# Kernel optimization log

Hardware: AMD Instinct MI355X
Metric: run time of the kernel (lower is better)

## Reference

```python
import jax, jax.numpy as jnp
import numpy as np

D_MODEL = 1024
N_HEADS = 16
DEPTH = D_MODEL // N_HEADS  # 64
BATCH, SEQ = 4, 2048


def setup_inputs() -> dict:
    key = jax.random.key(0)
    ks = jax.random.split(key, 8)
    x = jax.random.normal(ks[0], (BATCH, SEQ, D_MODEL), dtype=jnp.float32)
    # Per-head Dense(depth) weights stacked over heads: [H, d_model, depth]
    s = 1.0 / np.sqrt(D_MODEL)
    Wq = jax.random.normal(ks[1], (N_HEADS, D_MODEL, DEPTH), dtype=jnp.float32) * s
    Wk = jax.random.normal(ks[2], (N_HEADS, D_MODEL, DEPTH), dtype=jnp.float32) * s
    Wv = jax.random.normal(ks[3], (N_HEADS, D_MODEL, DEPTH), dtype=jnp.float32) * s
    bq = jnp.zeros((N_HEADS, DEPTH), dtype=jnp.float32)
    bk = jnp.zeros((N_HEADS, DEPTH), dtype=jnp.float32)
    bv = jnp.zeros((N_HEADS, DEPTH), dtype=jnp.float32)
    Wo = jax.random.normal(ks[4], (D_MODEL, D_MODEL), dtype=jnp.float32) * s
    bo = jnp.zeros((D_MODEL,), dtype=jnp.float32)
    return {"x": x, "Wq": Wq, "bq": bq, "Wk": Wk, "bk": bk,
            "Wv": Wv, "bv": bv, "Wo": Wo, "bo": bo}


def reference(x, Wq, bq, Wk, bk, Wv, bv, Wo, bo):
    # Per-head projections, batched over heads: [b, h, s, depth]
    q = jnp.einsum('bsd,hde->bhse', x, Wq) + bq[None, :, None, :]
    k = jnp.einsum('bsd,hde->bhse', x, Wk) + bk[None, :, None, :]
    v = jnp.einsum('bsd,hde->bhse', x, Wv) + bv[None, :, None, :]
    scale = 1.0 / jnp.sqrt(jnp.float32(DEPTH))
    scores = jnp.einsum('bhqe,bhke->bhqk', q, k) * scale  # [b, h, s, s]
    attn = jax.nn.softmax(scores, axis=-1)
    z = jnp.einsum('bhqk,bhke->bhqe', attn, v)  # [b, h, s, depth]
    # Concat heads along last axis (head-major order matches tf.concat of per-head outputs)
    multi_head = z.transpose(0, 2, 1, 3).reshape(BATCH, SEQ, D_MODEL)
    return multi_head @ Wo + bo
```

## Files before the change

kernel.cpp:

```cpp
#include <hip/hip_runtime.h>

typedef unsigned short u16;
typedef __bf16 bf16x8 __attribute__((ext_vector_type(8)));
typedef float f32x4 __attribute__((ext_vector_type(4)));
typedef float f32x16 __attribute__((ext_vector_type(16)));
typedef unsigned int u32x4 __attribute__((ext_vector_type(4)));
typedef unsigned int u32x2 __attribute__((ext_vector_type(2)));

__device__ __forceinline__ u16 f2b(float f) {
  union { float f; unsigned u; } v; v.f = f;
  return (u16)((v.u + 0x7fffu + ((v.u >> 16) & 1u)) >> 16);
}

__device__ __forceinline__ unsigned pkbf(float a, float b) {
#if __has_builtin(__builtin_amdgcn_cvt_pk_bf16_f32)
  typedef __bf16 bf16x2v __attribute__((ext_vector_type(2)));
  bf16x2v r = __builtin_amdgcn_cvt_pk_bf16_f32(a, b);
  return __builtin_bit_cast(unsigned, r);
#else
  unsigned ua = __builtin_bit_cast(unsigned, a) + 0x8000u;
  unsigned ub = __builtin_bit_cast(unsigned, b) + 0x8000u;
  return __builtin_amdgcn_perm(ub, ua, 0x07060302u);
#endif
}

__device__ __forceinline__ float fexp2(float x) {
#if __has_builtin(__builtin_amdgcn_exp2f)
  return __builtin_amdgcn_exp2f(x);
#else
  return exp2f(x);
#endif
}

__device__ __forceinline__ bf16x8 ldfrag(const u16* p) {
  u32x4 r = *(const u32x4*)p;
  return __builtin_bit_cast(bf16x8, r);
}

__device__ __forceinline__ void plswap(unsigned& dst, unsigned& src) {
  asm("v_permlane32_swap_b32 %0, %1" : "+v"(dst), "+v"(src));
}

__device__ __forceinline__ float sum16(const f32x16& v) {
  float a = (v[0] + v[1]) + (v[2] + v[3]);
  float b = (v[4] + v[5]) + (v[6] + v[7]);
  float c = (v[8] + v[9]) + (v[10] + v[11]);
  float d = (v[12] + v[13]) + (v[14] + v[15]);
  return (a + b) + (c + d);
}

__device__ __forceinline__ void build_frags(const f32x16& sc, bf16x8& fLo, bf16x8& fHi) {
  unsigned a0 = pkbf(sc[0], sc[1]);
  unsigned a1 = pkbf(sc[2], sc[3]);
  unsigned b0 = pkbf(sc[4], sc[5]);
  unsigned b1 = pkbf(sc[6], sc[7]);
  plswap(a0, b0);
  plswap(a1, b1);
  u32x4 f; f[0] = a0; f[1] = a1; f[2] = b0; f[3] = b1;
  fLo = __builtin_bit_cast(bf16x8, f);
  unsigned c0 = pkbf(sc[8], sc[9]);
  unsigned c1 = pkbf(sc[10], sc[11]);
  unsigned d0 = pkbf(sc[12], sc[13]);
  unsigned d1 = pkbf(sc[14], sc[15]);
  plswap(c0, d0);
  plswap(c1, d1);
  u32x4 g; g[0] = c0; g[1] = c1; g[2] = d0; g[3] = d1;
  fHi = __builtin_bit_cast(bf16x8, g);
}

#define GLOAD_LDS16(gp, lp)                                                        \
  __builtin_amdgcn_global_load_lds((const __attribute__((address_space(1))) void*)(gp), \
                                   (__attribute__((address_space(3))) void*)(lp), 16, 0, 0)

#define MFMA32(a, b, c) __builtin_amdgcn_mfma_f32_32x32x16_bf16((a), (b), (c), 0, 0, 0)

#define QSC 0.18033688011f


__global__ __launch_bounds__(256) void k_pack(const float* __restrict__ x,
                                              const float* __restrict__ Wq,
                                              const float* __restrict__ Wk,
                                              const float* __restrict__ Wv,
                                              const float* __restrict__ Wo,
                                              u16* __restrict__ xb,
                                              u16* __restrict__ wqkv,
                                              u16* __restrict__ wo_t) {
  const int bid = blockIdx.x, tid = threadIdx.x;
  if (bid < 4096) {
    int i = (bid * 256 + tid) * 8;
    float4 v0 = *(const float4*)(x + i);
    float4 v1 = *(const float4*)(x + i + 4);
    u32x4 o;
    o[0] = pkbf(v0.x, v0.y);
    o[1] = pkbf(v0.z, v0.w);
    o[2] = pkbf(v1.x, v1.y);
    o[3] = pkbf(v1.z, v1.w);
    *(u32x4*)(xb + i) = o;
    return;
  }
  __shared__ u16 tile[64][65];
  if (bid < 4864) {
    int b2 = bid - 4096;
    int p = b2 >> 8, rem = b2 & 255, h = rem >> 4, dt = rem & 15;
    const float* W = (p == 0) ? Wq : (p == 1) ? Wk : Wv;
    for (int i = tid; i < 4096; i += 256) {
      int d = i >> 6, e = i & 63;
      tile[e][d] = f2b(W[h * 65536 + (dt * 64 + d) * 64 + e]);
    }
    __syncthreads();
    for (int i = tid; i < 4096; i += 256) {
      int e = i >> 6, d = i & 63;
      wqkv[(size_t)(p * 1024 + h * 64 + e) * 1024 + dt * 64 + d] = tile[e][d];
    }
  } else {
    int b2 = bid - 4864;
    int kt = b2 >> 4, nt = b2 & 15;
    for (int i = tid; i < 4096; i += 256) {
      int dk = i >> 6, de = i & 63;
      tile[de][dk] = f2b(Wo[(size_t)(kt * 64 + dk) * 1024 + nt * 64 + de]);
    }
    __syncthreads();
    for (int i = tid; i < 4096; i += 256) {
      int de = i >> 6, dk = i & 63;
      wo_t[(size_t)(nt * 64 + de) * 1024 + kt * 64 + dk] = tile[de][dk];
    }
  }
}


template <bool SWAP>
__device__ __forceinline__ void gemm_core64(const u16* __restrict__ A, const u16* __restrict__ Bt,
                                            int row0, int col0, u16* As, u16* Bs, f32x16 acc[2][2]) {
  const int tid = threadIdx.x, w = tid >> 6, lane = tid & 63;
  const int l31 = lane & 31, hi = lane >> 5;
  const int wm = (w >> 1) * 64, wn = (w & 1) * 64;

  int r_[4], c_[4];
#pragma unroll
  for (int i = 0; i < 4; i++) {
    int E = (w * 4 + i) * 512 + lane * 8;
    int e = E ^ (((E >> 7) & 7) << 3);
    r_[i] = e >> 6;
    c_[i] = e & 63;
  }
  int oa[2][2][2], ob[2][2][2];
#pragma unroll
  for (int kh = 0; kh < 2; kh++)
#pragma unroll
    for (int t = 0; t < 2; t++)
#pragma unroll
      for (int s = 0; s < 2; s++) {
        int Pa = (wm + t * 32 + l31) * 64 + kh * 32 + s * 16 + hi * 8;
        int Pb = (wn + t * 32 + l31) * 64 + kh * 32 + s * 16 + hi * 8;
        oa[kh][t][s] = Pa ^ (((Pa >> 7) & 7) << 3);
        ob[kh][t][s] = Pb ^ (((Pb >> 7) & 7) << 3);
      }

  const u16* Ag = A + (size_t)row0 * 1024;
  const u16* Bg = Bt + (size_t)col0 * 1024;

#pragma unroll
  for (int i = 0; i < 4; i++) {
    GLOAD_LDS16(Ag + (size_t)r_[i] * 1024 + c_[i], As + (w * 4 + i) * 512);
    GLOAD_LDS16(Bg + (size_t)r_[i] * 1024 + c_[i], Bs + (w * 4 + i) * 512);
  }
  __syncthreads();

  int cur = 0;
  for (int k0 = 0; k0 < 1024; k0 += 64) {
    if (k0 + 64 < 1024) {
      u16* Ad = As + (cur ^ 1) * 8192 + (w * 4) * 512;
      u16* Bd = Bs + (cur ^ 1) * 8192 + (w * 4) * 512;
#pragma unroll
      for (int i = 0; i < 4; i++) {
        GLOAD_LDS16(Ag + (size_t)r_[i] * 1024 + k0 + 64 + c_[i], Ad + i * 512);
        GLOAD_LDS16(Bg + (size_t)r_[i] * 1024 + k0 + 64 + c_[i], Bd + i * 512);
      }
    }
    const u16* Ab = As + cur * 8192;
    const u16* Bb = Bs + cur * 8192;
#pragma unroll
    for (int kh = 0; kh < 2; kh++) {
      bf16x8 af[2][2], bfr[2][2];
#pragma unroll
      for (int t = 0; t < 2; t++)
#pragma unroll
        for (int s = 0; s < 2; s++) {
          af[t][s] = ldfrag(Ab + oa[kh][t][s]);
          bfr[t][s] = ldfrag(Bb + ob[kh][t][s]);
        }
      __builtin_amdgcn_s_setprio(1);
#pragma unroll
      for (int mt = 0; mt < 2; mt++)
#pragma unroll
        for (int nt = 0; nt < 2; nt++)
#pragma unroll
          for (int s = 0; s < 2; s++)
            acc[mt][nt] = SWAP ? MFMA32(bfr[nt][s], af[mt][s], acc[mt][nt])
                               : MFMA32(af[mt][s], bfr[nt][s], acc[mt][nt]);
      __builtin_amdgcn_s_setprio(0);
    }
    __syncthreads();
    cur ^= 1;
  }
}


__global__ __launch_bounds__(256) void k_gemm_qkv(const u16* __restrict__ xb, const u16* __restrict__ wt,
                                                  const float* __restrict__ bq, const float* __restrict__ bk,
                                                  const float* __restrict__ bv,
                                                  u16* __restrict__ qo, u16* __restrict__ ko,
                                                  u16* __restrict__ vto) {
  __shared__ u16 As[16384], Bs[16384];
  f32x16 acc[2][2];
#pragma unroll
  for (int a = 0; a < 2; a++)
#pragma unroll
    for (int b = 0; b < 2; b++)
#pragma unroll
      for (int r = 0; r < 16; r++) acc[a][b][r] = 0.f;

  const int row0 = blockIdx.x * 128, col0 = blockIdx.y * 128;
  const int p = blockIdx.y >> 3;
  const int colr = (blockIdx.y & 7) * 128;
  const int tid = threadIdx.x, w = tid >> 6, lane = tid & 63;
  const int l31 = lane & 31, hi = lane >> 5;
  const int wm = (w >> 1) * 64, wn = (w & 1) * 64;

  if (p == 2) {
    gemm_core64<true>(xb, wt, row0, col0, As, Bs, acc);
#pragma unroll
    for (int mt = 0; mt < 2; mt++) {
      int rb = row0 + wm + mt * 32;
      int b_ = rb >> 11;
      int s_ = (rb & 2047) + l31;
#pragma unroll
      for (int nt = 0; nt < 2; nt++) {
        int ebase = colr + wn + nt * 32;
#pragma unroll
        for (int g = 0; g < 4; g++) {
          float4 bvv = *(const float4*)(bv + ebase + g * 8 + hi * 4);
#pragma unroll
          for (int j = 0; j < 4; j++) {
            int rem = ebase + g * 8 + hi * 4 + j;
            int h = rem >> 6, e = rem & 63;
            float val = acc[mt][nt][g * 4 + j] + (&bvv.x)[j];
            vto[(((size_t)(b_ * 16 + h)) * 64 + e) * 2048 + s_] = f2b(val);
          }
        }
      }
    }
  } else {
    gemm_core64<false>(xb, wt, row0, col0, As, Bs, acc);
    u16* dst = (p == 0) ? qo : ko;
    const float* bias = (p == 0) ? bq : bk;
    const float qsc = (p == 0) ? QSC : 1.0f;
#pragma unroll
    for (int nt = 0; nt < 2; nt++) {
      int rem = colr + wn + nt * 32 + l31;
      int h = rem >> 6, e = rem & 63;
      float bval = bias[rem];
#pragma unroll
      for (int mt = 0; mt < 2; mt++) {
        int rb = row0 + wm + mt * 32;
        int b_ = rb >> 11, sb = rb & 2047;
        size_t obase = ((size_t)(b_ * 16 + h) * 2048) * 64 + e;
#pragma unroll
        for (int reg = 0; reg < 16; reg++) {
          int s_ = sb + (reg & 3) + 8 * (reg >> 2) + 4 * hi;
          float val = (acc[mt][nt][reg] + bval) * qsc;
          dst[obase + (size_t)s_ * 64] = f2b(val);
        }
      }
    }
  }
}


__global__ __launch_bounds__(256) void k_gemm_out(const u16* __restrict__ zb, const u16* __restrict__ wt,
                                                  const float* __restrict__ bo, float* __restrict__ out) {
  __shared__ u16 As[16384], Bs[16384];
  f32x16 acc[2][2];
#pragma unroll
  for (int a = 0; a < 2; a++)
#pragma unroll
    for (int b = 0; b < 2; b++)
#pragma unroll
      for (int r = 0; r < 16; r++) acc[a][b][r] = 0.f;

  const int row0 = blockIdx.x * 128, col0 = blockIdx.y * 128;
  gemm_core64<false>(zb, wt, row0, col0, As, Bs, acc);

  const int tid = threadIdx.x, w = tid >> 6, lane = tid & 63;
  const int l31 = lane & 31, hi = lane >> 5;
  const int wm = (w >> 1) * 64, wn = (w & 1) * 64;
#pragma unroll
  for (int nt = 0; nt < 2; nt++) {
    int c = col0 + wn + nt * 32 + l31;
    float bval = bo[c];
#pragma unroll
    for (int mt = 0; mt < 2; mt++) {
      int rb = row0 + wm + mt * 32;
#pragma unroll
      for (int reg = 0; reg < 16; reg++) {
        int r = rb + (reg & 3) + 8 * (reg >> 2) + 4 * hi;
        out[(size_t)r * 1024 + c] = acc[mt][nt][reg] + bval;
      }
    }
  }
}


__global__ __launch_bounds__(256, 2) void k_attn(const u16* __restrict__ q, const u16* __restrict__ k,
                                                 const u16* __restrict__ vt, u16* __restrict__ z) {
  __shared__ u16 Ks[2][64 * 72], Vs[2][64 * 72];
  const int tid = threadIdx.x, w = tid >> 6, lane = tid & 63;
  const int l31 = lane & 31, hi = lane >> 5;
  const int bh = blockIdx.x, s0 = blockIdx.y * 256;
  const size_t base = (size_t)bh * 2048 * 64;
  const int qrow0 = s0 + w * 64;

  bf16x8 qf[2][4];
#pragma unroll
  for (int u = 0; u < 2; u++) {
    const u16* qp = q + base + (size_t)(qrow0 + u * 32 + l31) * 64 + hi * 8;
#pragma unroll
    for (int ks = 0; ks < 4; ks++) qf[u][ks] = ldfrag(qp + ks * 16);
  }

  f32x16 accT[2][2];
  float ls[2] = {0.f, 0.f};
#pragma unroll
  for (int u = 0; u < 2; u++)
#pragma unroll
    for (int r = 0; r < 16; r++) { accT[u][0][r] = 0.f; accT[u][1][r] = 0.f; }

  const int srow = tid >> 3;
  const int scol = (tid & 7) * 8;
  const u16* kg = k + base;
  const u16* vg = vt + base;

  u32x4 kr0 = *(const u32x4*)(kg + (size_t)srow * 64 + scol);
  u32x4 kr1 = *(const u32x4*)(kg + (size_t)(srow + 32) * 64 + scol);
  u32x4 vr0 = *(const u32x4*)(vg + (size_t)srow * 2048 + scol);
  u32x4 vr1 = *(const u32x4*)(vg + (size_t)(srow + 32) * 2048 + scol);
  *(u32x4*)&Ks[0][srow * 72 + scol] = kr0;
  *(u32x4*)&Ks[0][(srow + 32) * 72 + scol] = kr1;
  *(u32x4*)&Vs[0][srow * 72 + scol] = vr0;
  *(u32x4*)&Vs[0][(srow + 32) * 72 + scol] = vr1;
  kr0 = *(const u32x4*)(kg + (size_t)(64 + srow) * 64 + scol);
  kr1 = *(const u32x4*)(kg + (size_t)(64 + srow + 32) * 64 + scol);
  vr0 = *(const u32x4*)(vg + (size_t)srow * 2048 + 64 + scol);
  vr1 = *(const u32x4*)(vg + (size_t)(srow + 32) * 2048 + 64 + scol);
  __syncthreads();

  for (int kc = 0; kc < 2048; kc += 64) {
    const int buf = (kc >> 6) & 1;
    const u16* Kb = &Ks[buf][0];
    const u16* Vb = &Vs[buf][0];

    bf16x8 pf[2][4];
#pragma unroll
    for (int t = 0; t < 2; t++) {
      f32x16 scA, scB;
#pragma unroll
      for (int r = 0; r < 16; r++) { scA[r] = 0.f; scB[r] = 0.f; }
      __builtin_amdgcn_s_setprio(1);
#pragma unroll
      for (int ks = 0; ks < 4; ks++) {
        bf16x8 kf = ldfrag(Kb + (t * 32 + l31) * 72 + ks * 16 + hi * 8);
        scA = MFMA32(kf, qf[0][ks], scA);
        scB = MFMA32(kf, qf[1][ks], scB);
      }
      __builtin_amdgcn_s_setprio(0);
#pragma unroll
      for (int r = 0; r < 16; r++) scA[r] = fexp2(scA[r]);
#pragma unroll
      for (int r = 0; r < 16; r++) scB[r] = fexp2(scB[r]);
      ls[0] += sum16(scA);
      ls[1] += sum16(scB);
      build_frags(scA, pf[0][2 * t], pf[0][2 * t + 1]);
      build_frags(scB, pf[1][2 * t], pf[1][2 * t + 1]);
    }

    if (kc + 64 < 2048) {
      *(u32x4*)&Ks[buf ^ 1][srow * 72 + scol] = kr0;
      *(u32x4*)&Ks[buf ^ 1][(srow + 32) * 72 + scol] = kr1;
      *(u32x4*)&Vs[buf ^ 1][srow * 72 + scol] = vr0;
      *(u32x4*)&Vs[buf ^ 1][(srow + 32) * 72 + scol] = vr1;
      if (kc + 128 < 2048) {
        int kn = kc + 128;
        kr0 = *(const u32x4*)(kg + (size_t)(kn + srow) * 64 + scol);
        kr1 = *(const u32x4*)(kg + (size_t)(kn + srow + 32) * 64 + scol);
        vr0 = *(const u32x4*)(vg + (size_t)srow * 2048 + kn + scol);
        vr1 = *(const u32x4*)(vg + (size_t)(srow + 32) * 2048 + kn + scol);
      }
    }

    __builtin_amdgcn_s_setprio(1);
#pragma unroll
    for (int ks = 0; ks < 4; ks++) {
      bf16x8 vf0 = ldfrag(Vb + (0 * 32 + l31) * 72 + ks * 16 + hi * 8);
      bf16x8 vf1 = ldfrag(Vb + (1 * 32 + l31) * 72 + ks * 16 + hi * 8);
      accT[0][0] = MFMA32(vf0, pf[0][ks], accT[0][0]);
      accT[0][1] = MFMA32(vf1, pf[0][ks], accT[0][1]);
      accT[1][0] = MFMA32(vf0, pf[1][ks], accT[1][0]);
      accT[1][1] = MFMA32(vf1, pf[1][ks], accT[1][1]);
    }
    __builtin_amdgcn_s_setprio(0);
    __syncthreads();
  }

  const int b_ = bh >> 4, h = bh & 15;
#pragma unroll
  for (int u = 0; u < 2; u++) {
    float l = ls[u];
    l += __shfl_xor(l, 32);
    float inv = 1.f / l;
    int qrow = qrow0 + u * 32 + l31;
    u16* zr = z + ((size_t)(b_ * 2048 + qrow)) * 1024 + h * 64;
#pragma unroll
    for (int et = 0; et < 2; et++)
#pragma unroll
      for (int rr = 0; rr < 16; rr += 2) {
        unsigned pkd = pkbf(accT[u][et][rr] * inv, accT[u][et][rr + 1] * inv);
        int e = et * 32 + (rr & 3) + 8 * (rr >> 2) + 4 * hi;
        *(unsigned*)&zr[e] = pkd;
      }
  }
}


extern "C" void kernel_launch(void* const* d_in, const int* in_sizes, int n_in,
                              void* d_out, int out_size, void* d_ws, size_t ws_size,
                              hipStream_t stream) {
  (void)in_sizes; (void)n_in; (void)out_size;
  const float* x  = (const float*)d_in[0];
  const float* Wq = (const float*)d_in[1];
  const float* bq = (const float*)d_in[2];
  const float* Wk = (const float*)d_in[3];
  const float* bk = (const float*)d_in[4];
  const float* Wv = (const float*)d_in[5];
  const float* bv = (const float*)d_in[6];
  const float* Wo = (const float*)d_in[7];
  const float* bo = (const float*)d_in[8];
  float* out = (float*)d_out;
  char* ws = (char*)d_ws;
  if (ws_size < 92274688u) return;

  u16* xb   = (u16*)(ws + 0);
  u16* wqkv = (u16*)(ws + 16777216);
  u16* wo_t = (u16*)(ws + 23068672);
  u16* qb   = (u16*)(ws + 25165824);
  u16* kb   = (u16*)(ws + 41943040);
  u16* vtb  = (u16*)(ws + 58720256);
  u16* zb   = (u16*)(ws + 75497472);

  k_pack<<<5120, 256, 0, stream>>>(x, Wq, Wk, Wv, Wo, xb, wqkv, wo_t);
  k_gemm_qkv<<<dim3(64, 24), 256, 0, stream>>>(xb, wqkv, bq, bk, bv, qb, kb, vtb);
  k_attn<<<dim3(64, 8), 256, 0, stream>>>(qb, kb, vtb, zb);
  k_gemm_out<<<dim3(64, 8), 256, 0, stream>>>(zb, wo_t, bo, out);
}
```

Baseline: 269.7 us.

## Stage K/V via direct global-to-LDS loads with pre-swizzled layout and 128-key tiles

The QKV projection now writes Q, K and transposed V with an XOR swizzle baked into global memory. The attention kernel can then copy K/V tiles straight into LDS with global-load-to-LDS instructions, with no padding and no register staging. The key tile grows from 64 to 128 per barrier, which halves the number of syncs and doubles LDS use to 64KB per block. This is meant to cut VGPR pressure, LDS store instructions and bank conflicts, but it may reduce occupancy and depends on the GLOAD_LDS16 macro defined elsewhere.

```diff
diff --git a/kernel.cpp b/kernel.cpp
--- a/kernel.cpp
+++ b/kernel.cpp
@@ -244,8 +244,9 @@
           for (int j = 0; j < 4; j++) {
             int rem = ebase + g * 8 + hi * 4 + j;
             int h = rem >> 6, e = rem & 63;
+            int e7 = (hi * 4 + j) & 7;
             float val = acc[mt][nt][g * 4 + j] + (&bvv.x)[j];
-            vto[(((size_t)(b_ * 16 + h)) * 64 + e) * 2048 + s_] = f2b(val);
+            vto[((size_t)(b_ * 16 + h) * 64 + e) * 2048 + (s_ ^ (e7 << 3))] = f2b(val);
           }
         }
       }
@@ -264,12 +265,14 @@
       for (int mt = 0; mt < 2; mt++) {
         int rb = row0 + wm + mt * 32;
         int b_ = rb >> 11, sb = rb & 2047;
-        size_t obase = ((size_t)(b_ * 16 + h) * 2048) * 64 + e;
+        size_t base2 = (size_t)(b_ * 16 + h) * 2048 * 64;
 #pragma unroll
         for (int reg = 0; reg < 16; reg++) {
-          int s_ = sb + (reg & 3) + 8 * (reg >> 2) + 4 * hi;
+          int low = (reg & 3) + 4 * hi + 8 * (reg >> 2);
+          int s_ = sb + low;
+          int esw = e ^ ((((low >> 1) & 7)) << 3);
           float val = (acc[mt][nt][reg] + bval) * qsc;
-          dst[obase + (size_t)s_ * 64] = f2b(val);
+          dst[base2 + (size_t)s_ * 64 + esw] = f2b(val);
         }
       }
     }
@@ -313,19 +316,21 @@
 
 __global__ __launch_bounds__(256, 2) void k_attn(const u16* __restrict__ q, const u16* __restrict__ k,
                                                  const u16* __restrict__ vt, u16* __restrict__ z) {
-  __shared__ u16 Ks[2][64 * 72], Vs[2][64 * 72];
+  __shared__ u16 Ks[2][128 * 64], Vs[2][64 * 128];
   const int tid = threadIdx.x, w = tid >> 6, lane = tid & 63;
   const int l31 = lane & 31, hi = lane >> 5;
   const int bh = blockIdx.x, s0 = blockIdx.y * 256;
   const size_t base = (size_t)bh * 2048 * 64;
   const int qrow0 = s0 + w * 64;
+  const int qx = ((l31 >> 1) & 7) << 3;
+  const int vx = (l31 & 7) << 3;
 
   bf16x8 qf[2][4];
 #pragma unroll
   for (int u = 0; u < 2; u++) {
-    const u16* qp = q + base + (size_t)(qrow0 + u * 32 + l31) * 64 + hi * 8;
-#pragma unroll
-    for (int ks = 0; ks < 4; ks++) qf[u][ks] = ldfrag(qp + ks * 16);
+    const u16* qp = q + base + (size_t)(qrow0 + u * 32 + l31) * 64;
+#pragma unroll
+    for (int ks = 0; ks < 4; ks++) qf[u][ks] = ldfrag(qp + ((ks * 16 + hi * 8) ^ qx));
   }
 
   f32x16 accT[2][2];
@@ -335,81 +340,70 @@
 #pragma unroll
     for (int r = 0; r < 16; r++) { accT[u][0][r] = 0.f; accT[u][1][r] = 0.f; }
 
-  const int srow = tid >> 3;
-  const int scol = (tid & 7) * 8;
   const u16* kg = k + base;
   const u16* vg = vt + base;
 
-  u32x4 kr0 = *(const u32x4*)(kg + (size_t)srow * 64 + scol);
-  u32x4 kr1 = *(const u32x4*)(kg + (size_t)(srow + 32) * 64 + scol);
-  u32x4 vr0 = *(const u32x4*)(vg + (size_t)srow * 2048 + scol);
-  u32x4 vr1 = *(const u32x4*)(vg + (size_t)(srow + 32) * 2048 + scol);
-  *(u32x4*)&Ks[0][srow * 72 + scol] = kr0;
-  *(u32x4*)&Ks[0][(srow + 32) * 72 + scol] = kr1;
-  *(u32x4*)&Vs[0][srow * 72 + scol] = vr0;
-  *(u32x4*)&Vs[0][(srow + 32) * 72 + scol] = vr1;
-  kr0 = *(const u32x4*)(kg + (size_t)(64 + srow) * 64 + scol);
-  kr1 = *(const u32x4*)(kg + (size_t)(64 + srow + 32) * 64 + scol);
-  vr0 = *(const u32x4*)(vg + (size_t)srow * 2048 + 64 + scol);
-  vr1 = *(const u32x4*)(vg + (size_t)(srow + 32) * 2048 + 64 + scol);
+#define STAGE_KV(buf, kc)                                                                  \
+  {                                                                                        \
+    _Pragma("unroll") for (int i = 0; i < 4; i++) {                                        \
+      int g = w * 256 + i * 64 + lane;                                                     \
+      GLOAD_LDS16(kg + (size_t)((kc) + (g >> 3)) * 64 + (g & 7) * 8,                       \
+                  &Ks[buf][(w * 256 + i * 64) * 8]);                                       \
+      GLOAD_LDS16(vg + (size_t)(g >> 4) * 2048 + (kc) + (g & 15) * 8,                      \
+                  &Vs[buf][(w * 256 + i * 64) * 8]);                                       \
+    }                                                                                      \
+  }
+
+  STAGE_KV(0, 0);
   __syncthreads();
 
-  for (int kc = 0; kc < 2048; kc += 64) {
-    const int buf = (kc >> 6) & 1;
+  for (int kc = 0; kc < 2048; kc += 128) {
+    const int buf = (kc >> 7) & 1;
+    if (kc + 128 < 2048) STAGE_KV(buf ^ 1, kc + 128);
     const u16* Kb = &Ks[buf][0];
     const u16* Vb = &Vs[buf][0];
 
-    bf16x8 pf[2][4];
-#pragma unroll
-    for (int t = 0; t < 2; t++) {
-      f32x16 scA, scB;
-#pragma unroll
-      for (int r = 0; r < 16; r++) { scA[r] = 0.f; scB[r] = 0.f; }
+#pragma unroll
+    for (int sc = 0; sc < 2; sc++) {
+      bf16x8 pf[2][4];
+#pragma unroll
+      for (int t = 0; t < 2; t++) {
+        f32x16 scA, scB;
+#pragma unroll
+        for (int r = 0; r < 16; r++) { scA[r] = 0.f; scB[r] = 0.f; }
+        __builtin_amdgcn_s_setprio(1);
+#pragma unroll
+        for (int ks = 0; ks < 4; ks++) {
+          bf16x8 kf = ldfrag(Kb + (sc * 64 + t * 32 + l31) * 64 + ((ks * 16 + hi * 8) ^ qx));
+          scA = MFMA32(kf, qf[0][ks], scA);
+          scB = MFMA32(kf, qf[1][ks], scB);
+        }
+        __builtin_amdgcn_s_setprio(0);
+#pragma unroll
+        for (int r = 0; r < 16; r++) scA[r] = fexp2(scA[r]);
+#pragma unroll
+        for (int r = 0; r < 16; r++) scB[r] = fexp2(scB[r]);
+        ls[0] += sum16(scA);
+        ls[1] += sum16(scB);
+        build_frags(scA, pf[0][2 * t], pf[0][2 * t + 1]);
+        build_frags(scB, pf[1][2 * t], pf[1][2 * t + 1]);
+      }
+
       __builtin_amdgcn_s_setprio(1);
 #pragma unroll
       for (int ks = 0; ks < 4; ks++) {
-        bf16x8 kf = ldfrag(Kb + (t * 32 + l31) * 72 + ks * 16 + hi * 8);
-        scA = MFMA32(kf, qf[0][ks], scA);
-        scB = MFMA32(kf, qf[1][ks], scB);
+        bf16x8 vf0 = ldfrag(Vb + (0 * 32 + l31) * 128 + ((sc * 64 + ks * 16 + hi * 8) ^ vx));
+        bf16x8 vf1 = ldfrag(Vb + (1 * 32 + l31) * 128 + ((sc * 64 + ks * 16 + hi * 8) ^ vx));
+        accT[0][0] = MFMA32(vf0, pf[0][ks], accT[0][0]);
+        accT[0][1] = MFMA32(vf1, pf[0][ks], accT[0][1]);
+        accT[1][0] = MFMA32(vf0, pf[1][ks], accT[1][0]);
+        accT[1][1] = MFMA32(vf1, pf[1][ks], accT[1][1]);
       }
       __builtin_amdgcn_s_setprio(0);
-#pragma unroll
-      for (int r = 0; r < 16; r++) scA[r] = fexp2(scA[r]);
-#pragma unroll
-      for (int r = 0; r < 16; r++) scB[r] = fexp2(scB[r]);
-      ls[0] += sum16(scA);
-      ls[1] += sum16(scB);
-      build_frags(scA, pf[0][2 * t], pf[0][2 * t + 1]);
-      build_frags(scB, pf[1][2 * t], pf[1][2 * t + 1]);
-    }
-
-    if (kc + 64 < 2048) {
-      *(u32x4*)&Ks[buf ^ 1][srow * 72 + scol] = kr0;
-      *(u32x4*)&Ks[buf ^ 1][(srow + 32) * 72 + scol] = kr1;
-      *(u32x4*)&Vs[buf ^ 1][srow * 72 + scol] = vr0;
-      *(u32x4*)&Vs[buf ^ 1][(srow + 32) * 72 + scol] = vr1;
-      if (kc + 128 < 2048) {
-        int kn = kc + 128;
-        kr0 = *(const u32x4*)(kg + (size_t)(kn + srow) * 64 + scol);
-        kr1 = *(const u32x4*)(kg + (size_t)(kn + srow + 32) * 64 + scol);
-        vr0 = *(const u32x4*)(vg + (size_t)srow * 2048 + kn + scol);
-        vr1 = *(const u32x4*)(vg + (size_t)(srow + 32) * 2048 + kn + scol);
-      }
-    }
-
-    __builtin_amdgcn_s_setprio(1);
-#pragma unroll
-    for (int ks = 0; ks < 4; ks++) {
-      bf16x8 vf0 = ldfrag(Vb + (0 * 32 + l31) * 72 + ks * 16 + hi * 8);
-      bf16x8 vf1 = ldfrag(Vb + (1 * 32 + l31) * 72 + ks * 16 + hi * 8);
-      accT[0][0] = MFMA32(vf0, pf[0][ks], accT[0][0]);
-      accT[0][1] = MFMA32(vf1, pf[0][ks], accT[0][1]);
-      accT[1][0] = MFMA32(vf0, pf[1][ks], accT[1][0]);
-      accT[1][1] = MFMA32(vf1, pf[1][ks], accT[1][1]);
-    }
-    __builtin_amdgcn_s_setprio(0);
+    }
     __syncthreads();
   }
+#undef STAGE_KV
 
   const int b_ = bh >> 4, h = bh & 15;
 #pragma unroll
```

New measurement: 360.9 us. 1.34x slower.
